# Performance work log

Hardware: AMD Instinct MI355X
Metric: run time of the kernel (lower is better)

The kernel has to match this reference:

```python
import jax, jax.numpy as jnp
import numpy as np

C = 256
NUM_HEADS = 8
GROUPS = 8
EPS = 1e-5


def setup_inputs() -> dict:
    key = jax.random.key(0)
    ks = jax.random.split(key, 7)
    B, H, W = 2, 64, 64
    x = jax.random.normal(ks[0], (B, C, H, W), dtype=jnp.float32)
    gn_weight = jnp.ones((C,), dtype=jnp.float32)
    gn_bias = jnp.zeros((C,), dtype=jnp.float32)
    # 1x1 convs == per-pixel linear layers
    w_qkv = jax.random.normal(ks[1], (3 * C, C), dtype=jnp.float32) * (1.0 / np.sqrt(C))
    b_qkv = jax.random.normal(ks[2], (3 * C,), dtype=jnp.float32) * 0.01
    w_proj = jax.random.normal(ks[3], (C, C), dtype=jnp.float32) * (1.0 / np.sqrt(C))
    b_proj = jax.random.normal(ks[4], (C,), dtype=jnp.float32) * 0.01
    return {"x": x, "gn_weight": gn_weight, "gn_bias": gn_bias,
            "w_qkv": w_qkv, "b_qkv": b_qkv, "w_proj": w_proj, "b_proj": b_proj}


def reference(x, gn_weight, gn_bias, w_qkv, b_qkv, w_proj, b_proj):
    B, Cc, H, W = x.shape
    nh = NUM_HEADS
    hd = Cc // nh
    N = H * W
    scale = hd ** (-0.5)

    # GroupNorm(8, C): normalize over (C/G, H, W) per group, biased variance
    xg = x.reshape(B, GROUPS, Cc // GROUPS, H, W)
    mean = xg.mean(axis=(2, 3, 4), keepdims=True)
    var = xg.var(axis=(2, 3, 4), keepdims=True)
    hn = (xg - mean) * jax.lax.rsqrt(var + EPS)
    hn = hn.reshape(B, Cc, H, W) * gn_weight[None, :, None, None] + gn_bias[None, :, None, None]

    hf = hn.reshape(B, Cc, N)                       # [B, C, N]
    qkv = jnp.einsum('oc,bcn->bon', w_qkv, hf) + b_qkv[None, :, None]  # [B, 3C, N]
    qkv = qkv.reshape(B, 3, nh, hd, N)
    # q,k,v: [B, nh, N, hd]
    q = jnp.transpose(qkv[:, 0], (0, 1, 3, 2))
    k = jnp.transpose(qkv[:, 1], (0, 1, 3, 2))
    v = jnp.transpose(qkv[:, 2], (0, 1, 3, 2))

    attn = jnp.einsum('bhqd,bhkd->bhqk', q, k) * scale  # [B, nh, N, N]
    attn = jax.nn.softmax(attn, axis=-1)
    o = jnp.einsum('bhqk,bhkd->bhqd', attn, v)           # [B, nh, N, hd]
    o = jnp.transpose(o, (0, 1, 3, 2)).reshape(B, Cc, H, W)

    of = o.reshape(B, Cc, N)
    out = jnp.einsum('oc,bcn->bon', w_proj, of) + b_proj[None, :, None]
    return out.reshape(B, Cc, H, W)
```

## Files before the change

kernel.cpp:

```cpp
#include <hip/hip_runtime.h>


typedef _Float16 half8 __attribute__((ext_vector_type(8)));
typedef __fp16   fp16x2 __attribute__((ext_vector_type(2)));
typedef float    f32x4 __attribute__((ext_vector_type(4)));
typedef int      int2v __attribute__((ext_vector_type(2)));
typedef int      int4v __attribute__((ext_vector_type(4)));

__device__ __forceinline__ f32x4 mfma16(half8 a, half8 b, f32x4 c) {
  return __builtin_amdgcn_mfma_f32_16x16x32_f16(a, b, c, 0, 0, 0);
}

#if __has_builtin(__builtin_amdgcn_exp2f)
#define EXP2(x) __builtin_amdgcn_exp2f(x)
#else
#define EXP2(x) exp2f(x)
#endif

__device__ __forceinline__ unsigned short h_bits(_Float16 h) {
  return __builtin_bit_cast(unsigned short, h);
}
__device__ __forceinline__ int h2_bits(fp16x2 h) {
  return __builtin_bit_cast(int, h);
}

constexpr float CSCALE = (float)(1.4426950408889634 / 5.656854249492381);
constexpr float LOSC   = 2048.0f;
constexpr float ILOSC  = 1.0f / 2048.0f;

__global__ __launch_bounds__(256) void gn_stats(const float* __restrict__ x,
                                                float* __restrict__ stats) {
  const int bg = blockIdx.x, ch = blockIdx.y, tid = threadIdx.x;
  const float* p = x + (size_t)bg * 131072 + (size_t)ch * 4096;
  float s = 0.f, ss = 0.f;
#pragma unroll
  for (int j = 0; j < 4; ++j) {
    f32x4 v = *(const f32x4*)(p + j * 1024 + tid * 4);
#pragma unroll
    for (int k = 0; k < 4; ++k) { s += v[k]; ss += v[k] * v[k]; }
  }
#pragma unroll
  for (int m = 1; m <= 32; m <<= 1) { s += __shfl_xor(s, m); ss += __shfl_xor(ss, m); }
  __shared__ float red[8];
  const int wv = tid >> 6;
  if ((tid & 63) == 0) { red[wv * 2] = s; red[wv * 2 + 1] = ss; }
  __syncthreads();
  if (tid == 0) {
    float S = red[0] + red[2] + red[4] + red[6];
    float SS = red[1] + red[3] + red[5] + red[7];
    atomicAdd(&stats[bg * 2], S);
    atomicAdd(&stats[bg * 2 + 1], SS);
  }
}

__global__ __launch_bounds__(256) void gn_apply(const float* __restrict__ x,
                                                const float* __restrict__ gw,
                                                const float* __restrict__ gb,
                                                const float* __restrict__ stats,
                                                _Float16* __restrict__ hn_hi,
                                                _Float16* __restrict__ hn_lo) {
  __shared__ float tile[64 * 65];
  const int tid = threadIdx.x;
  const int a = tid & 15;
  const int row16 = tid >> 4;
  const int b = blockIdx.z, c0 = blockIdx.y * 64, n0 = blockIdx.x * 64;
#pragma unroll
  for (int m = 0; m < 4; ++m) {
    const int cl = row16 + 16 * m;
    const int c = c0 + cl;
    const int g = c >> 5;
    const float s = stats[(b * 8 + g) * 2];
    const float ss = stats[(b * 8 + g) * 2 + 1];
    const float mean = s * (1.f / 131072.f);
    const float var = ss * (1.f / 131072.f) - mean * mean;
    const float rstd = rsqrtf(var + 1e-5f);
    const float ga = gw[c] * rstd;
    const float be = gb[c] - mean * ga;
    f32x4 xv = *(const f32x4*)(x + ((size_t)(b * 256 + c)) * 4096 + n0 + a * 4);
#pragma unroll
    for (int j = 0; j < 4; ++j) tile[cl * 65 + a * 4 + j] = xv[j] * ga + be;
  }
  __syncthreads();
#pragma unroll
  for (int m = 0; m < 4; ++m) {
    const int nl = row16 + 16 * m;
    const int cb = a * 4;
    unsigned short hh[4], ll[4];
#pragma unroll
    for (int j = 0; j < 4; ++j) {
      float v = tile[(cb + j) * 65 + nl];
      _Float16 h = (_Float16)v;
      hh[j] = h_bits(h);
      ll[j] = h_bits((_Float16)((v - (float)h) * LOSC));
    }
    int2v uh, ul;
    uh[0] = hh[0] | (hh[1] << 16); uh[1] = hh[2] | (hh[3] << 16);
    ul[0] = ll[0] | (ll[1] << 16); ul[1] = ll[2] | (ll[3] << 16);
    size_t off = ((size_t)(b * 4096 + n0 + nl)) * 256 + c0 + cb;
    *(int2v*)(hn_hi + off) = uh;
    *(int2v*)(hn_lo + off) = ul;
  }
}

__global__ __launch_bounds__(256) void wsplit(const float* __restrict__ wq,
                                              const float* __restrict__ wp,
                                              _Float16* __restrict__ wqh,
                                              _Float16* __restrict__ wql,
                                              _Float16* __restrict__ wph,
                                              _Float16* __restrict__ wpl) {
  const int idx = blockIdx.x * 256 + threadIdx.x;
  if (idx < 196608) {
    float v = wq[idx];
    _Float16 h = (_Float16)v;
    wqh[idx] = h;
    wql[idx] = (_Float16)((v - (float)h) * LOSC);
  } else {
    const int i2 = idx - 196608;
    float v = wp[i2];
    _Float16 h = (_Float16)v;
    wph[i2] = h;
    wpl[i2] = (_Float16)((v - (float)h) * LOSC);
  }
}

template <int MODE>
__global__ __launch_bounds__(256) void gemm_split(
    const _Float16* __restrict__ Ahi, const _Float16* __restrict__ Alo,
    const _Float16* __restrict__ Bhi, const _Float16* __restrict__ Blo,
    const float* __restrict__ bias,
    _Float16* __restrict__ qkT, _Float16* __restrict__ v_t,
    float* __restrict__ outp) {
  __shared__ _Float16 a_lds[8192];
  __shared__ _Float16 b_lds[8192];
  const int tid = threadIdx.x, lane = tid & 63, wv = tid >> 6;
  const int qq = lane >> 4, ii = lane & 15;
  const int m0 = blockIdx.x * 64, n0 = blockIdx.y * 64, bz = blockIdx.z;
  const int hlT = (tid >> 7) & 1, cT = (tid >> 6) & 1;
  const int qT = (tid >> 4) & 3, iT = tid & 15;
  const _Float16* Asel = hlT ? Alo : Ahi;
  const _Float16* Bsel = hlT ? Blo : Bhi;
  const _Float16* aptr = Asel + (size_t)(m0 + iT) * 256 + 32 * cT + 8 * qT;
  const _Float16* bptr = Bsel + ((size_t)(bz * 4096 + n0 + iT)) * 256 + 32 * cT + 8 * qT;

  f32x4 acc[4] = {}, acc2[4] = {};
  for (int k0 = 0; k0 < 256; k0 += 64) {
#pragma unroll
    for (int j = 0; j < 4; ++j) {
      *(half8*)(a_lds + (((j * 2 + hlT) * 2 + cT) * 64 + (tid & 63)) * 8) =
          *(const half8*)(aptr + (size_t)(16 * j) * 256 + k0);
      *(half8*)(b_lds + (((j * 2 + hlT) * 2 + cT) * 64 + (tid & 63)) * 8) =
          *(const half8*)(bptr + (size_t)(16 * j) * 256 + k0);
    }
    __syncthreads();
    half8 ah[2], al[2];
#pragma unroll
    for (int c = 0; c < 2; ++c) {
      ah[c] = *(const half8*)(a_lds + (((wv * 2 + 0) * 2 + c) * 64 + lane) * 8);
      al[c] = *(const half8*)(a_lds + (((wv * 2 + 1) * 2 + c) * 64 + lane) * 8);
    }
#pragma unroll
    for (int t = 0; t < 4; ++t) {
#pragma unroll
      for (int c = 0; c < 2; ++c) {
        half8 bh_ = *(const half8*)(b_lds + (((t * 2 + 0) * 2 + c) * 64 + lane) * 8);
        half8 bl_ = *(const half8*)(b_lds + (((t * 2 + 1) * 2 + c) * 64 + lane) * 8);
        acc[t]  = mfma16(ah[c], bh_, acc[t]);
        acc2[t] = mfma16(ah[c], bl_, acc2[t]);
        acc2[t] = mfma16(al[c], bh_, acc2[t]);
      }
    }
    __syncthreads();
  }

  const int och0 = m0 + 16 * wv + 4 * qq;
  if (MODE == 0) {
    if (m0 < 512) {
      const float sc = (m0 < 256) ? CSCALE : 1.0f;
#pragma unroll
      for (int t = 0; t < 4; ++t) {
        const int n = n0 + 16 * t + ii;
        unsigned short hh[4];
#pragma unroll
        for (int r = 0; r < 4; ++r) {
          float val = (acc[t][r] + acc2[t][r] * ILOSC + bias[och0 + r]) * sc;
          hh[r] = h_bits((_Float16)val);
        }
        int2v u;
        u[0] = hh[0] | (hh[1] << 16);
        u[1] = hh[2] | (hh[3] << 16);
        *(int2v*)(qkT + ((size_t)(bz * 4096 + n)) * 512 + och0) = u;
      }
    } else {
#pragma unroll
      for (int t = 0; t < 4; ++t) {
#pragma unroll
        for (int r = 0; r < 4; ++r) {
          const int och = och0 + r;
          const int d = och - 512;
          const int hd_ = d & 31, head = d >> 5;
          const int n = n0 + 16 * t + ii;
          float val = acc[t][r] + acc2[t][r] * ILOSC + bias[och];
          v_t[((size_t)((bz * 8 + head) * 32 + hd_)) * 4096 + n] = (_Float16)val;
        }
      }
    }
  } else {
#pragma unroll
    for (int t = 0; t < 4; ++t) {
#pragma unroll
      for (int r = 0; r < 4; ++r) {
        const int och = och0 + r;
        const int n = n0 + 16 * t + ii;
        outp[((size_t)(bz * 256 + och)) * 4096 + n] =
            acc[t][r] + acc2[t][r] * ILOSC + bias[och];
      }
    }
  }
}

__global__ __launch_bounds__(256) void attn_kernel(
    const _Float16* __restrict__ qkT, const _Float16* __restrict__ v_t,
    float* __restrict__ opart, float* __restrict__ lpart) {
  __shared__ _Float16 k_lds[2][4096];
  __shared__ _Float16 v_lds[2][4096];
  const int tid = threadIdx.x, lane = tid & 63, wv = tid >> 6;
  const int qq = lane >> 4, ii = lane & 15;
  const int bh = blockIdx.y, b = bh >> 3, h = bh & 7;
  const int n0 = blockIdx.x * 128;
  const int part = blockIdx.z;
  const int key0 = part * 2048;

  const _Float16* qbase =
      qkT + ((size_t)(b * 4096 + n0 + 32 * wv + ii)) * 512 + h * 32 + 8 * qq;
  half8 qf0 = *(const half8*)qbase;
  half8 qf1 = *(const half8*)(qbase + (size_t)16 * 512);

  const _Float16* ksrc[2];
  const _Float16* vsrc[2];
  int dst8[2];
#pragma unroll
  for (int rep = 0; rep < 2; ++rep) {
    const int idx = tid + 256 * rep;
    dst8[rep] = idx * 8;
    const int f = idx >> 6, l = idx & 63;
    const int fq = l >> 4, fi = l & 15;
    const int u = f >> 1, hf = f & 1;
    const int g = 32 * u + 4 * hf + 8 * (fi >> 2) + (fi & 3);
    ksrc[rep] = qkT + ((size_t)(b * 4096 + key0 + g)) * 512 + 256 + h * 32 + 8 * fq;
    vsrc[rep] = v_t + ((size_t)(bh * 32 + 16 * hf + fi)) * 4096 + key0 + 32 * u + 8 * fq;
  }

  half8 ones8;
#pragma unroll
  for (int j = 0; j < 8; ++j) ones8[j] = (_Float16)1.0f;

  f32x4 o00 = {}, o10 = {}, o01 = {}, o11 = {}, accl0 = {}, accl1 = {};

  half8 kr0 = *(const half8*)ksrc[0];
  half8 kr1 = *(const half8*)ksrc[1];
  half8 vr0 = *(const half8*)vsrc[0];
  half8 vr1 = *(const half8*)vsrc[1];
  *(half8*)(k_lds[0] + dst8[0]) = kr0;
  *(half8*)(k_lds[0] + dst8[1]) = kr1;
  *(half8*)(v_lds[0] + dst8[0]) = vr0;
  *(half8*)(v_lds[0] + dst8[1]) = vr1;
  __syncthreads();

  for (int kb = 0; kb < 16; ++kb) {
    const int cur = kb & 1;
    if (kb < 15) {
      const size_t ko = (size_t)(kb + 1) * 128 * 512;
      const size_t vo = (size_t)(kb + 1) * 128;
      kr0 = *(const half8*)(ksrc[0] + ko);
      kr1 = *(const half8*)(ksrc[1] + ko);
      vr0 = *(const half8*)(vsrc[0] + vo);
      vr1 = *(const half8*)(vsrc[1] + vo);
    }
    const _Float16* kbase = k_lds[cur];
    const _Float16* vbase = v_lds[cur];

#pragma unroll
    for (int u = 0; u < 4; ++u) {
      half8 kfa = *(const half8*)(kbase + u * 1024 + lane * 8);
      half8 kfb = *(const half8*)(kbase + u * 1024 + 512 + lane * 8);
      f32x4 z = {};
      f32x4 sa0 = mfma16(kfa, qf0, z);
      f32x4 sb0 = mfma16(kfb, qf0, z);
      f32x4 sa1 = mfma16(kfa, qf1, z);
      f32x4 sb1 = mfma16(kfb, qf1, z);
      int4v p0, p1;
      p0[0] = h2_bits(__builtin_amdgcn_cvt_pkrtz(EXP2(sa0[0]), EXP2(sa0[1])));
      p0[1] = h2_bits(__builtin_amdgcn_cvt_pkrtz(EXP2(sa0[2]), EXP2(sa0[3])));
      p0[2] = h2_bits(__builtin_amdgcn_cvt_pkrtz(EXP2(sb0[0]), EXP2(sb0[1])));
      p0[3] = h2_bits(__builtin_amdgcn_cvt_pkrtz(EXP2(sb0[2]), EXP2(sb0[3])));
      p1[0] = h2_bits(__builtin_amdgcn_cvt_pkrtz(EXP2(sa1[0]), EXP2(sa1[1])));
      p1[1] = h2_bits(__builtin_amdgcn_cvt_pkrtz(EXP2(sa1[2]), EXP2(sa1[3])));
      p1[2] = h2_bits(__builtin_amdgcn_cvt_pkrtz(EXP2(sb1[0]), EXP2(sb1[1])));
      p1[3] = h2_bits(__builtin_amdgcn_cvt_pkrtz(EXP2(sb1[2]), EXP2(sb1[3])));
      half8 pt0 = __builtin_bit_cast(half8, p0);
      half8 pt1 = __builtin_bit_cast(half8, p1);
      half8 vf0 = *(const half8*)(vbase + u * 1024 + lane * 8);
      half8 vf1 = *(const half8*)(vbase + u * 1024 + 512 + lane * 8);
      o00 = mfma16(vf0, pt0, o00);
      o10 = mfma16(vf1, pt0, o10);
      accl0 = mfma16(ones8, pt0, accl0);
      o01 = mfma16(vf0, pt1, o01);
      o11 = mfma16(vf1, pt1, o11);
      accl1 = mfma16(ones8, pt1, accl1);
    }

    if (kb < 15) {
      _Float16* kn = k_lds[cur ^ 1];
      _Float16* vn = v_lds[cur ^ 1];
      *(half8*)(kn + dst8[0]) = kr0;
      *(half8*)(kn + dst8[1]) = kr1;
      *(half8*)(vn + dst8[0]) = vr0;
      *(half8*)(vn + dst8[1]) = vr1;
    }
    __syncthreads();
  }

#pragma unroll
  for (int hf = 0; hf < 2; ++hf) {
    const f32x4 oa = hf ? o01 : o00;
    const f32x4 ob = hf ? o11 : o10;
    const int q = n0 + 32 * wv + 16 * hf + ii;
    float* base = opart + ((size_t)((part * 2 + b) * 4096 + q)) * 256 + h * 32;
    *(f32x4*)(base + 4 * qq) = oa;
    *(f32x4*)(base + 16 + 4 * qq) = ob;
    if (qq == 0) {
      lpart[((size_t)((part * 2 + b) * 4096 + q)) * 8 + h] = hf ? accl1[0] : accl0[0];
    }
  }
}

__global__ __launch_bounds__(256) void attn_combine(
    const float* __restrict__ opart, const float* __restrict__ lpart,
    _Float16* __restrict__ o_hi, _Float16* __restrict__ o_lo) {
  const int c = threadIdx.x, hh = c >> 5;
#pragma unroll
  for (int k = 0; k < 4; ++k) {
    const int row = blockIdx.x * 4 + k;
    const int b = row >> 12;
    const size_t i0 = ((size_t)(0 * 2 + b) * 4096 + (row & 4095)) * 256 + c;
    const size_t i1 = ((size_t)(1 * 2 + b) * 4096 + (row & 4095)) * 256 + c;
    const size_t l0i = ((size_t)(0 * 2 + b) * 4096 + (row & 4095)) * 8 + hh;
    const size_t l1i = ((size_t)(1 * 2 + b) * 4096 + (row & 4095)) * 8 + hh;
    const float O = opart[i0] + opart[i1];
    const float inv = 1.0f / (lpart[l0i] + lpart[l1i]);
    const float v = O * inv;
    _Float16 hv = (_Float16)v;
    const size_t out = (size_t)row * 256 + c;
    o_hi[out] = hv;
    o_lo[out] = (_Float16)((v - (float)hv) * LOSC);
  }
}

extern "C" void kernel_launch(void* const* d_in, const int* in_sizes, int n_in,
                              void* d_out, int out_size, void* d_ws, size_t ws_size,
                              hipStream_t stream) {
  const float* x     = (const float*)d_in[0];
  const float* gnw   = (const float*)d_in[1];
  const float* gnb   = (const float*)d_in[2];
  const float* wqkv  = (const float*)d_in[3];
  const float* bqkv  = (const float*)d_in[4];
  const float* wproj = (const float*)d_in[5];
  const float* bproj = (const float*)d_in[6];
  float* out = (float*)d_out;

  char* ws = (char*)d_ws;
  size_t off = 0;
  auto alloc = [&](size_t bytes) -> char* {
    char* p = ws + off;
    off += (bytes + 255) & ~(size_t)255;
    return p;
  };
  float*    stats  = (float*)alloc(128);
  _Float16* hn_hi  = (_Float16*)alloc((size_t)2 * 4096 * 256 * 2);
  _Float16* hn_lo  = (_Float16*)alloc((size_t)2 * 4096 * 256 * 2);
  _Float16* wq_hi  = (_Float16*)alloc((size_t)768 * 256 * 2);
  _Float16* wq_lo  = (_Float16*)alloc((size_t)768 * 256 * 2);
  _Float16* wp_hi  = (_Float16*)alloc((size_t)256 * 256 * 2);
  _Float16* wp_lo  = (_Float16*)alloc((size_t)256 * 256 * 2);
  _Float16* qkT    = (_Float16*)alloc((size_t)2 * 4096 * 512 * 2);
  _Float16* v_t    = (_Float16*)alloc((size_t)16 * 32 * 4096 * 2);
  float*    opart  = (float*)alloc((size_t)4 * 4096 * 256 * 4);
  float*    lpart  = (float*)alloc((size_t)4 * 4096 * 8 * 4);
  _Float16* o_hi = hn_hi;
  _Float16* o_lo = hn_lo;
  if (off > ws_size) return;

  (void)hipMemsetAsync(stats, 0, 256, stream);
  gn_stats<<<dim3(16, 32), 256, 0, stream>>>(x, stats);
  gn_apply<<<dim3(64, 4, 2), 256, 0, stream>>>(x, gnw, gnb, stats, hn_hi, hn_lo);
  wsplit<<<1024, 256, 0, stream>>>(wqkv, wproj, wq_hi, wq_lo, wp_hi, wp_lo);
  gemm_split<0><<<dim3(12, 64, 2), 256, 0, stream>>>(wq_hi, wq_lo, hn_hi, hn_lo,
                                                     bqkv, qkT, v_t, nullptr);
  attn_kernel<<<dim3(32, 16, 2), 256, 0, stream>>>(qkT, v_t, opart, lpart);
  attn_combine<<<2048, 256, 0, stream>>>(opart, lpart, o_hi, o_lo);
  gemm_split<1><<<dim3(4, 64, 2), 256, 0, stream>>>(wp_hi, wp_lo, o_hi, o_lo,
                                                    bproj, nullptr, nullptr, out);
}
```

Baseline: 178.2 us.

## Drop hi/lo fp16 split for single fp16 GEMMs with double-buffered LDS

Removes the error-compensating hi/lo fp16 split used for the QKV and projection GEMMs and their inputs, so each GEMM issues one MFMA per tile instead of three and moves half the input bytes. gn_apply, the weight cast and attn_combine now write only a single fp16 buffer. The GEMM main loop is also restructured to double-buffer LDS, prefetching the next K-slice into registers while the current one is computed. This lowers numerical accuracy of the projections to plain fp16, which may matter against the fp32 reference tolerance.

Result: faster. 162.8 us (-8.6%).

```diff
diff --git a/kernel.cpp b/kernel.cpp
--- a/kernel.cpp
+++ b/kernel.cpp
@@ -25,8 +25,6 @@
 }
 
 constexpr float CSCALE = (float)(1.4426950408889634 / 5.656854249492381);
-constexpr float LOSC   = 2048.0f;
-constexpr float ILOSC  = 1.0f / 2048.0f;
 
 __global__ __launch_bounds__(256) void gn_stats(const float* __restrict__ x,
                                                 float* __restrict__ stats) {
@@ -57,8 +55,7 @@
                                                 const float* __restrict__ gw,
                                                 const float* __restrict__ gb,
                                                 const float* __restrict__ stats,
-                                                _Float16* __restrict__ hn_hi,
-                                                _Float16* __restrict__ hn_lo) {
+                                                _Float16* __restrict__ hn) {
   __shared__ float tile[64 * 65];
   const int tid = threadIdx.x;
   const int a = tid & 15;
@@ -85,89 +82,92 @@
   for (int m = 0; m < 4; ++m) {
     const int nl = row16 + 16 * m;
     const int cb = a * 4;
-    unsigned short hh[4], ll[4];
+    int2v uh;
+    unsigned short hh[4];
 #pragma unroll
     for (int j = 0; j < 4; ++j) {
-      float v = tile[(cb + j) * 65 + nl];
-      _Float16 h = (_Float16)v;
-      hh[j] = h_bits(h);
-      ll[j] = h_bits((_Float16)((v - (float)h) * LOSC));
-    }
-    int2v uh, ul;
+      hh[j] = h_bits((_Float16)tile[(cb + j) * 65 + nl]);
+    }
     uh[0] = hh[0] | (hh[1] << 16); uh[1] = hh[2] | (hh[3] << 16);
-    ul[0] = ll[0] | (ll[1] << 16); ul[1] = ll[2] | (ll[3] << 16);
     size_t off = ((size_t)(b * 4096 + n0 + nl)) * 256 + c0 + cb;
-    *(int2v*)(hn_hi + off) = uh;
-    *(int2v*)(hn_lo + off) = ul;
-  }
-}
-
-__global__ __launch_bounds__(256) void wsplit(const float* __restrict__ wq,
-                                              const float* __restrict__ wp,
-                                              _Float16* __restrict__ wqh,
-                                              _Float16* __restrict__ wql,
-                                              _Float16* __restrict__ wph,
-                                              _Float16* __restrict__ wpl) {
+    *(int2v*)(hn + off) = uh;
+  }
+}
+
+__global__ __launch_bounds__(256) void wcast(const float* __restrict__ wq,
+                                             const float* __restrict__ wp,
+                                             _Float16* __restrict__ wqh,
+                                             _Float16* __restrict__ wph) {
   const int idx = blockIdx.x * 256 + threadIdx.x;
   if (idx < 196608) {
-    float v = wq[idx];
-    _Float16 h = (_Float16)v;
-    wqh[idx] = h;
-    wql[idx] = (_Float16)((v - (float)h) * LOSC);
+    wqh[idx] = (_Float16)wq[idx];
   } else {
-    const int i2 = idx - 196608;
-    float v = wp[i2];
-    _Float16 h = (_Float16)v;
-    wph[i2] = h;
-    wpl[i2] = (_Float16)((v - (float)h) * LOSC);
+    wph[idx - 196608] = (_Float16)wp[idx - 196608];
   }
 }
 
 template <int MODE>
-__global__ __launch_bounds__(256) void gemm_split(
-    const _Float16* __restrict__ Ahi, const _Float16* __restrict__ Alo,
-    const _Float16* __restrict__ Bhi, const _Float16* __restrict__ Blo,
+__global__ __launch_bounds__(256) void gemm_f16(
+    const _Float16* __restrict__ W, const _Float16* __restrict__ Bm,
     const float* __restrict__ bias,
     _Float16* __restrict__ qkT, _Float16* __restrict__ v_t,
     float* __restrict__ outp) {
-  __shared__ _Float16 a_lds[8192];
-  __shared__ _Float16 b_lds[8192];
+  __shared__ _Float16 a_lds[2][4096];
+  __shared__ _Float16 b_lds[2][4096];
   const int tid = threadIdx.x, lane = tid & 63, wv = tid >> 6;
   const int qq = lane >> 4, ii = lane & 15;
   const int m0 = blockIdx.x * 64, n0 = blockIdx.y * 64, bz = blockIdx.z;
-  const int hlT = (tid >> 7) & 1, cT = (tid >> 6) & 1;
-  const int qT = (tid >> 4) & 3, iT = tid & 15;
-  const _Float16* Asel = hlT ? Alo : Ahi;
-  const _Float16* Bsel = hlT ? Blo : Bhi;
-  const _Float16* aptr = Asel + (size_t)(m0 + iT) * 256 + 32 * cT + 8 * qT;
-  const _Float16* bptr = Bsel + ((size_t)(bz * 4096 + n0 + iT)) * 256 + 32 * cT + 8 * qT;
-
-  f32x4 acc[4] = {}, acc2[4] = {};
-  for (int k0 = 0; k0 < 256; k0 += 64) {
-#pragma unroll
-    for (int j = 0; j < 4; ++j) {
-      *(half8*)(a_lds + (((j * 2 + hlT) * 2 + cT) * 64 + (tid & 63)) * 8) =
-          *(const half8*)(aptr + (size_t)(16 * j) * 256 + k0);
-      *(half8*)(b_lds + (((j * 2 + hlT) * 2 + cT) * 64 + (tid & 63)) * 8) =
-          *(const half8*)(bptr + (size_t)(16 * j) * 256 + k0);
-    }
-    __syncthreads();
-    half8 ah[2], al[2];
-#pragma unroll
-    for (int c = 0; c < 2; ++c) {
-      ah[c] = *(const half8*)(a_lds + (((wv * 2 + 0) * 2 + c) * 64 + lane) * 8);
-      al[c] = *(const half8*)(a_lds + (((wv * 2 + 1) * 2 + c) * 64 + lane) * 8);
-    }
+
+  const _Float16* asrc[2];
+  const _Float16* bsrc[2];
+  int dst8[2];
+#pragma unroll
+  for (int rep = 0; rep < 2; ++rep) {
+    const int idx = tid + 256 * rep;
+    dst8[rep] = idx * 8;
+    const int j = idx >> 7, c = (idx >> 6) & 1, l = idx & 63;
+    const int lq = l >> 4, li = l & 15;
+    asrc[rep] = W + (size_t)(m0 + 16 * j + li) * 256 + 32 * c + 8 * lq;
+    bsrc[rep] = Bm + ((size_t)(bz * 4096 + n0 + 16 * j + li)) * 256 + 32 * c + 8 * lq;
+  }
+
+  f32x4 acc[4] = {};
+
+  half8 ar0 = *(const half8*)asrc[0];
+  half8 ar1 = *(const half8*)asrc[1];
+  half8 br0 = *(const half8*)bsrc[0];
+  half8 br1 = *(const half8*)bsrc[1];
+  *(half8*)(a_lds[0] + dst8[0]) = ar0;
+  *(half8*)(a_lds[0] + dst8[1]) = ar1;
+  *(half8*)(b_lds[0] + dst8[0]) = br0;
+  *(half8*)(b_lds[0] + dst8[1]) = br1;
+  __syncthreads();
+
+  for (int it = 0; it < 4; ++it) {
+    const int cur = it & 1;
+    if (it < 3) {
+      const int ko = (it + 1) * 64;
+      ar0 = *(const half8*)(asrc[0] + ko);
+      ar1 = *(const half8*)(asrc[1] + ko);
+      br0 = *(const half8*)(bsrc[0] + ko);
+      br1 = *(const half8*)(bsrc[1] + ko);
+    }
+    half8 ah0 = *(const half8*)(a_lds[cur] + ((wv * 2 + 0) * 64 + lane) * 8);
+    half8 ah1 = *(const half8*)(a_lds[cur] + ((wv * 2 + 1) * 64 + lane) * 8);
 #pragma unroll
     for (int t = 0; t < 4; ++t) {
-#pragma unroll
-      for (int c = 0; c < 2; ++c) {
-        half8 bh_ = *(const half8*)(b_lds + (((t * 2 + 0) * 2 + c) * 64 + lane) * 8);
-        half8 bl_ = *(const half8*)(b_lds + (((t * 2 + 1) * 2 + c) * 64 + lane) * 8);
-        acc[t]  = mfma16(ah[c], bh_, acc[t]);
-        acc2[t] = mfma16(ah[c], bl_, acc2[t]);
-        acc2[t] = mfma16(al[c], bh_, acc2[t]);
-      }
+      half8 b0 = *(const half8*)(b_lds[cur] + ((t * 2 + 0) * 64 + lane) * 8);
+      half8 b1 = *(const half8*)(b_lds[cur] + ((t * 2 + 1) * 64 + lane) * 8);
+      acc[t] = mfma16(ah0, b0, acc[t]);
+      acc[t] = mfma16(ah1, b1, acc[t]);
+    }
+    if (it < 3) {
+      _Float16* an = a_lds[cur ^ 1];
+      _Float16* bn = b_lds[cur ^ 1];
+      *(half8*)(an + dst8[0]) = ar0;
+      *(half8*)(an + dst8[1]) = ar1;
+      *(half8*)(bn + dst8[0]) = br0;
+      *(half8*)(bn + dst8[1]) = br1;
     }
     __syncthreads();
   }
@@ -182,8 +182,7 @@
         unsigned short hh[4];
 #pragma unroll
         for (int r = 0; r < 4; ++r) {
-          float val = (acc[t][r] + acc2[t][r] * ILOSC + bias[och0 + r]) * sc;
-          hh[r] = h_bits((_Float16)val);
+          hh[r] = h_bits((_Float16)((acc[t][r] + bias[och0 + r]) * sc));
         }
         int2v u;
         u[0] = hh[0] | (hh[1] << 16);
@@ -199,8 +198,8 @@
           const int d = och - 512;
           const int hd_ = d & 31, head = d >> 5;
           const int n = n0 + 16 * t + ii;
-          float val = acc[t][r] + acc2[t][r] * ILOSC + bias[och];
-          v_t[((size_t)((bz * 8 + head) * 32 + hd_)) * 4096 + n] = (_Float16)val;
+          v_t[((size_t)((bz * 8 + head) * 32 + hd_)) * 4096 + n] =
+              (_Float16)(acc[t][r] + bias[och]);
         }
       }
     }
@@ -211,8 +210,7 @@
       for (int r = 0; r < 4; ++r) {
         const int och = och0 + r;
         const int n = n0 + 16 * t + ii;
-        outp[((size_t)(bz * 256 + och)) * 4096 + n] =
-            acc[t][r] + acc2[t][r] * ILOSC + bias[och];
+        outp[((size_t)(bz * 256 + och)) * 4096 + n] = acc[t][r] + bias[och];
       }
     }
   }
@@ -336,7 +334,7 @@
 
 __global__ __launch_bounds__(256) void attn_combine(
     const float* __restrict__ opart, const float* __restrict__ lpart,
-    _Float16* __restrict__ o_hi, _Float16* __restrict__ o_lo) {
+    _Float16* __restrict__ o16) {
   const int c = threadIdx.x, hh = c >> 5;
 #pragma unroll
   for (int k = 0; k < 4; ++k) {
@@ -348,11 +346,7 @@
     const size_t l1i = ((size_t)(1 * 2 + b) * 4096 + (row & 4095)) * 8 + hh;
     const float O = opart[i0] + opart[i1];
     const float inv = 1.0f / (lpart[l0i] + lpart[l1i]);
-    const float v = O * inv;
-    _Float16 hv = (_Float16)v;
-    const size_t out = (size_t)row * 256 + c;
-    o_hi[out] = hv;
-    o_lo[out] = (_Float16)((v - (float)hv) * LOSC);
+    o16[(size_t)row * 256 + c] = (_Float16)(O * inv);
   }
 }
 
@@ -376,28 +370,24 @@
     return p;
   };
   float*    stats  = (float*)alloc(128);
-  _Float16* hn_hi  = (_Float16*)alloc((size_t)2 * 4096 * 256 * 2);
-  _Float16* hn_lo  = (_Float16*)alloc((size_t)2 * 4096 * 256 * 2);
-  _Float16* wq_hi  = (_Float16*)alloc((size_t)768 * 256 * 2);
-  _Float16* wq_lo  = (_Float16*)alloc((size_t)768 * 256 * 2);
-  _Float16* wp_hi  = (_Float16*)alloc((size_t)256 * 256 * 2);
-  _Float16* wp_lo  = (_Float16*)alloc((size_t)256 * 256 * 2);
+  _Float16* hn     = (_Float16*)alloc((size_t)2 * 4096 * 256 * 2);
+  _Float16* wq_h   = (_Float16*)alloc((size_t)768 * 256 * 2);
+  _Float16* wp_h   = (_Float16*)alloc((size_t)256 * 256 * 2);
   _Float16* qkT    = (_Float16*)alloc((size_t)2 * 4096 * 512 * 2);
   _Float16* v_t    = (_Float16*)alloc((size_t)16 * 32 * 4096 * 2);
   float*    opart  = (float*)alloc((size_t)4 * 4096 * 256 * 4);
   float*    lpart  = (float*)alloc((size_t)4 * 4096 * 8 * 4);
-  _Float16* o_hi = hn_hi;
-  _Float16* o_lo = hn_lo;
+  _Float16* o16 = hn;
   if (off > ws_size) return;
 
   (void)hipMemsetAsync(stats, 0, 256, stream);
   gn_stats<<<dim3(16, 32), 256, 0, stream>>>(x, stats);
-  gn_apply<<<dim3(64, 4, 2), 256, 0, stream>>>(x, gnw, gnb, stats, hn_hi, hn_lo);
-  wsplit<<<1024, 256, 0, stream>>>(wqkv, wproj, wq_hi, wq_lo, wp_hi, wp_lo);
-  gemm_split<0><<<dim3(12, 64, 2), 256, 0, stream>>>(wq_hi, wq_lo, hn_hi, hn_lo,
-                                                     bqkv, qkT, v_t, nullptr);
+  gn_apply<<<dim3(64, 4, 2), 256, 0, stream>>>(x, gnw, gnb, stats, hn);
+  wcast<<<1024, 256, 0, stream>>>(wqkv, wproj, wq_h, wp_h);
+  gemm_f16<0><<<dim3(12, 64, 2), 256, 0, stream>>>(wq_h, hn, bqkv, qkT, v_t,
+                                                   nullptr);
   attn_kernel<<<dim3(32, 16, 2), 256, 0, stream>>>(qkT, v_t, opart, lpart);
-  attn_combine<<<2048, 256, 0, stream>>>(opart, lpart, o_hi, o_lo);
-  gemm_split<1><<<dim3(4, 64, 2), 256, 0, stream>>>(wp_hi, wp_lo, o_hi, o_lo,
-                                                    bproj, nullptr, nullptr, out);
-}
+  attn_combine<<<2048, 256, 0, stream>>>(opart, lpart, o16);
+  gemm_f16<1><<<dim3(4, 64, 2), 256, 0, stream>>>(wp_h, o16, bproj, nullptr,
+                                                  nullptr, out);
+}
```
